# Performance work log

Hardware: AMD Instinct MI355X
Metric: run time of the kernel (lower is better)

The kernel has to match this reference:

```python
import jax, jax.numpy as jnp
import numpy as np
from jax import lax

V, E, H, S, B = 32000, 150, 30, 128, 32
STDV = 1.0 / np.sqrt(30.0)


def setup_inputs() -> dict:
    key = jax.random.key(0)
    ks = jax.random.split(key, 9)
    u = lambda k, shape: jax.random.uniform(k, shape, jnp.float32, -STDV, STDV)
    return {
        "input_batch": jax.random.randint(ks[0], (S, B), 0, V),
        "embedding": u(ks[1], (V, E)),
        "W_ih_lr": u(ks[2], (E + H, H)),
        "b_ih_lr": u(ks[3], (1, H)),
        "W_ih_rl": u(ks[4], (E + H, H)),
        "b_ih_rl": u(ks[5], (1, H)),
        "W_ho": u(ks[6], (2 * H, V)),
        "b_ho": u(ks[7], (1, V)),
        "initial_hidden": u(ks[8], (1, H)),
    }


def reference(input_batch, embedding, W_ih_lr, b_ih_lr, W_ih_rl, b_ih_rl,
              W_ho, b_ho, initial_hidden):
    seq_len, batch = input_batch.shape
    emb = embedding[input_batch]  # (S, B, E)
    # original code detaches the initial hidden state (uses .data)
    init = jnp.broadcast_to(lax.stop_gradient(initial_hidden), (batch, initial_hidden.shape[1]))

    def step(W, b):
        def f(h, w):
            h_new = jnp.tanh(jnp.concatenate([w, h], axis=1) @ W + b)
            return h_new, h_new
        return f

    # forward (left-to-right): f_states[t] = hLR[t+1]
    _, f_states = lax.scan(step(W_ih_lr, b_ih_lr), init, emb)
    # backward (right-to-left) over reversed tokens: r_states[k] = hRL[S-1-k]
    _, r_states = lax.scan(step(W_ih_rl, b_ih_rl), init, emb[::-1])

    # prediction at i uses hLR[i] and hRL[i+1]
    hLR_used = jnp.concatenate([init[None], f_states[:-1]], axis=0)        # hLR[0..S-1]
    hRL_used = jnp.concatenate([r_states[:-1][::-1], init[None]], axis=0)  # hRL[1..S]

    h_cat = jnp.concatenate([hLR_used, hRL_used], axis=-1)  # (S, B, 2H)
    logits = jnp.einsum('sbh,hv->sbv', h_cat, W_ho) + b_ho  # (S, B, V)
    return jax.nn.log_softmax(logits, axis=-1)
```

## Files before the change

kernel.cpp:

```cpp
#include <hip/hip_runtime.h>

#define VSZ 32000
#define ESZ 150
#define HSZ 30
#define SSZ 128
#define BSZ 32
#define SB  4096
#define KP  64

typedef __attribute__((ext_vector_type(8))) short bf16x8;
typedef __attribute__((ext_vector_type(4))) float f32x4;
typedef __attribute__((ext_vector_type(8))) unsigned short u16x8;

static __device__ __forceinline__ unsigned short f2bf(float f) {
  unsigned int u = __float_as_uint(f);
  u += 0x7fffu + ((u >> 16) & 1u);
  return (unsigned short)(u >> 16);
}

static __device__ __forceinline__ float readlane_f(float v, int lane) {
  return __uint_as_float(__builtin_amdgcn_readlane(__float_as_uint(v), lane));
}

__global__ void k_zproj(const int* __restrict__ idx, const float* __restrict__ emb,
                        const float* __restrict__ Wlr, const float* __restrict__ blr,
                        const float* __restrict__ Wrl, const float* __restrict__ brl,
                        float* __restrict__ z) {
  __shared__ float erow[ESZ];
  int tb = blockIdx.x;
  int row = idx[tb];
  for (int i = threadIdx.x; i < ESZ; i += 64) erow[i] = emb[row * ESZ + i];
  __syncthreads();
  int lane = threadIdx.x;
  int j = lane & 31, dir = lane >> 5;
  if (j < HSZ) {
    const float* W = dir ? Wrl : Wlr;
    float acc = dir ? brl[j] : blr[j];
#pragma unroll 10
    for (int e = 0; e < ESZ; ++e) acc = fmaf(erow[e], W[e * HSZ + j], acc);
    z[(dir * SB + tb) * HSZ + j] = acc;
  }
}

__global__ void k_scan(const float* __restrict__ z, const float* __restrict__ Wlr,
                       const float* __restrict__ Wrl, const float* __restrict__ h0,
                       unsigned short* __restrict__ hcat) {
  int j = threadIdx.x;
  int chain = blockIdx.x;
  int dir = chain >> 5, b = chain & 31;
  const float* W = dir ? Wrl : Wlr;
  float w2[HSZ];
#pragma unroll
  for (int k = 0; k < HSZ; ++k) w2[k] = (j < HSZ) ? W[(ESZ + k) * HSZ + j] : 0.f;
  float h = (j < HSZ) ? h0[j] : 0.f;
  bool wr = (j < 32);
  int dim = (j < HSZ) ? dir * HSZ + j : (dir ? 60 : 62) + (j - 30);
  unsigned short padbits = (dim == 60) ? f2bf(1.0f) : (unsigned short)0;
  const float* zc = z + dir * (SB * HSZ) + b * HSZ + j;
  int te0 = dir ? (SSZ - 1) : 0;
  float zv = (j < HSZ) ? zc[te0 * (BSZ * HSZ)] : 0.f;
  for (int t = 0; t < SSZ; ++t) {
    int te = dir ? (SSZ - 1 - t) : t;
    float zn = 0.f;
    if (t < SSZ - 1) {
      int ten = dir ? (SSZ - 2 - t) : (t + 1);
      zn = (j < HSZ) ? zc[ten * (BSZ * HSZ)] : 0.f;
    }
    int r = te * BSZ + b;
    if (wr) hcat[r * KP + dim] = (j < HSZ) ? f2bf(h) : padbits;
    float a0 = zv, a1 = 0.f, a2 = 0.f, a3 = 0.f;
#pragma unroll
    for (int k = 0; k < 28; k += 4) {
      a0 = fmaf(readlane_f(h, k),     w2[k],     a0);
      a1 = fmaf(readlane_f(h, k + 1), w2[k + 1], a1);
      a2 = fmaf(readlane_f(h, k + 2), w2[k + 2], a2);
      a3 = fmaf(readlane_f(h, k + 3), w2[k + 3], a3);
    }
    a0 = fmaf(readlane_f(h, 28), w2[28], a0);
    a1 = fmaf(readlane_f(h, 29), w2[29], a1);
    float x = (a0 + a1) + (a2 + a3);
    float e = __expf(2.0f * x);
    h = 1.0f - __fdividef(2.0f, e + 1.0f);
    zv = zn;
  }
}

__global__ void k_wprep(const float* __restrict__ Who, const float* __restrict__ bho,
                        unsigned short* __restrict__ Wbt) {
  int v = blockIdx.x * 256 + threadIdx.x;
  int kq = blockIdx.y;
  u16x8 pack;
#pragma unroll
  for (int i = 0; i < 8; ++i) {
    int k = kq * 8 + i;
    float val = (k < 60) ? Who[k * VSZ + v] : ((k == 60) ? bho[v] : 0.f);
    pack[i] = f2bf(val);
  }
  *(u16x8*)&Wbt[v * KP + kq * 8] = pack;
}

__global__ void k_sumexp(const unsigned short* __restrict__ hcat,
                         const unsigned short* __restrict__ Wbt,
                         float* __restrict__ part) {
  int mb = blockIdx.x, nb = blockIdx.y;
  int wave = threadIdx.x >> 6, lane = threadIdx.x & 63;
  int g = lane >> 4, c = lane & 15;
  int rbase = mb * 128 + wave * 32;
  bf16x8 bfr[2][2];
#pragma unroll
  for (int rg = 0; rg < 2; ++rg)
#pragma unroll
    for (int ks = 0; ks < 2; ++ks)
      bfr[rg][ks] = *(const bf16x8*)&hcat[(rbase + rg * 16 + c) * KP + ks * 32 + g * 8];
  float se[2] = {0.f, 0.f};
  int c0 = nb * 2000;
  for (int nt = 0; nt < 125; ++nt) {
    int ct = c0 + nt * 16;
    bf16x8 a0 = *(const bf16x8*)&Wbt[(ct + c) * KP + g * 8];
    bf16x8 a1 = *(const bf16x8*)&Wbt[(ct + c) * KP + 32 + g * 8];
#pragma unroll
    for (int rg = 0; rg < 2; ++rg) {
      f32x4 acc = {0.f, 0.f, 0.f, 0.f};
      acc = __builtin_amdgcn_mfma_f32_16x16x32_bf16(a0, bfr[rg][0], acc, 0, 0, 0);
      acc = __builtin_amdgcn_mfma_f32_16x16x32_bf16(a1, bfr[rg][1], acc, 0, 0, 0);
      se[rg] += (__expf(acc[0]) + __expf(acc[1])) + (__expf(acc[2]) + __expf(acc[3]));
    }
  }
#pragma unroll
  for (int rg = 0; rg < 2; ++rg) {
    se[rg] += __shfl_xor(se[rg], 16);
    se[rg] += __shfl_xor(se[rg], 32);
  }
  if (g == 0) {
#pragma unroll
    for (int rg = 0; rg < 2; ++rg)
      part[(rbase + rg * 16 + c) * 16 + nb] = se[rg];
  }
}

__global__ __launch_bounds__(256) void k_writeout(
    const unsigned short* __restrict__ hcat,
    const unsigned short* __restrict__ Wbt,
    const float* __restrict__ part,
    float* __restrict__ out) {
  __shared__ float Lsh[64];
  __shared__ float slab[4][16 * 64];
  int mb = blockIdx.x, nb = blockIdx.y;
  int tid = threadIdx.x;
  if (tid < 64) {
    const float* p = &part[(mb * 64 + tid) * 16];
    float s = 0.f;
#pragma unroll
    for (int k = 0; k < 16; ++k) s += p[k];
    Lsh[tid] = logf(s);
  }
  __syncthreads();
  int wave = tid >> 6, lane = tid & 63;
  int g = lane >> 4, c = lane & 15;
  int row0 = mb * 64 + wave * 16;
  bf16x8 b0f = *(const bf16x8*)&hcat[(row0 + c) * KP + g * 8];
  bf16x8 b1f = *(const bf16x8*)&hcat[(row0 + c) * KP + 32 + g * 8];
  float L = Lsh[wave * 16 + c];
  float* tl = slab[wave];
  int c0 = nb * 2000;
  for (int gq = 0; gq < 31; ++gq) {
    int ct0 = c0 + gq * 64;
#pragma unroll
    for (int t = 0; t < 4; ++t) {
      int ct = ct0 + t * 16;
      bf16x8 a0 = *(const bf16x8*)&Wbt[(ct + c) * KP + g * 8];
      bf16x8 a1 = *(const bf16x8*)&Wbt[(ct + c) * KP + 32 + g * 8];
      f32x4 acc = {0.f, 0.f, 0.f, 0.f};
      acc = __builtin_amdgcn_mfma_f32_16x16x32_bf16(a0, b0f, acc, 0, 0, 0);
      acc = __builtin_amdgcn_mfma_f32_16x16x32_bf16(a1, b1f, acc, 0, 0, 0);
      f32x4 v;
#pragma unroll
      for (int i = 0; i < 4; ++i) v[i] = acc[i] - L;
      int P = (t * 4 + g) ^ (c & 7);
      *(f32x4*)&tl[c * 64 + P * 4] = v;
    }
#pragma unroll
    for (int j = 0; j < 4; ++j) {
      int rj = 4 * j + g;
      int P = c ^ (rj & 7);
      f32x4 w = *(f32x4*)&tl[rj * 64 + P * 4];
      __builtin_nontemporal_store(w, (f32x4*)&out[(row0 + rj) * VSZ + ct0 + c * 4]);
    }
  }
  {
    int ct = c0 + 1984;
    bf16x8 a0 = *(const bf16x8*)&Wbt[(ct + c) * KP + g * 8];
    bf16x8 a1 = *(const bf16x8*)&Wbt[(ct + c) * KP + 32 + g * 8];
    f32x4 acc = {0.f, 0.f, 0.f, 0.f};
    acc = __builtin_amdgcn_mfma_f32_16x16x32_bf16(a0, b0f, acc, 0, 0, 0);
    acc = __builtin_amdgcn_mfma_f32_16x16x32_bf16(a1, b1f, acc, 0, 0, 0);
    f32x4 v;
#pragma unroll
    for (int i = 0; i < 4; ++i) v[i] = acc[i] - L;
    *(f32x4*)&out[(row0 + c) * VSZ + ct + g * 4] = v;
  }
}

extern "C" void kernel_launch(void* const* d_in, const int* in_sizes, int n_in,
                              void* d_out, int out_size, void* d_ws, size_t ws_size,
                              hipStream_t stream) {
  (void)in_sizes; (void)n_in; (void)out_size; (void)ws_size;
  const int*   idx = (const int*)d_in[0];
  const float* emb = (const float*)d_in[1];
  const float* Wlr = (const float*)d_in[2];
  const float* blr = (const float*)d_in[3];
  const float* Wrl = (const float*)d_in[4];
  const float* brl = (const float*)d_in[5];
  const float* Who = (const float*)d_in[6];
  const float* bho = (const float*)d_in[7];
  const float* h0  = (const float*)d_in[8];
  float* out = (float*)d_out;

  char* ws = (char*)d_ws;
  float*          z    = (float*)(ws + 0);
  unsigned short* hcat = (unsigned short*)(ws + 983040);
  unsigned short* Wbt  = (unsigned short*)(ws + 1507328);
  float*          part = (float*)(ws + 5603328);

  k_zproj<<<SB, 64, 0, stream>>>(idx, emb, Wlr, blr, Wrl, brl, z);
  k_scan<<<64, 64, 0, stream>>>(z, Wlr, Wrl, h0, hcat);
  k_wprep<<<dim3(125, 8), 256, 0, stream>>>(Who, bho, Wbt);
  k_sumexp<<<dim3(32, 16), 256, 0, stream>>>(hcat, Wbt, part);
  k_writeout<<<dim3(64, 16), 256, 0, stream>>>(hcat, Wbt, part, out);
}
```

Baseline: 274.9 us.

## Fuse sum-exp and writeout kernels with per-row-block atomic grid barrier

Merges the log-sum-exp partial pass and the output writeout into one kernel. The 16 column blocks that share a row block publish their partial sums and then spin on an atomic counter until all have arrived. Each block then reuses its register-held hcat fragments to recompute the logits and write the outputs. This removes one kernel launch and the reload of hcat. The cost is a cross-block spin wait that relies on all 16 cooperating blocks being resident at once (512 blocks, 2 per CU via launch bounds), plus a small extra kernel to zero the counters.

```diff
diff --git a/kernel.cpp b/kernel.cpp
--- a/kernel.cpp
+++ b/kernel.cpp
@@ -20,6 +20,10 @@
 
 static __device__ __forceinline__ float readlane_f(float v, int lane) {
   return __uint_as_float(__builtin_amdgcn_readlane(__float_as_uint(v), lane));
+}
+
+__global__ void k_zeroflags(int* __restrict__ cnt) {
+  if (threadIdx.x < 32) cnt[threadIdx.x] = 0;
 }
 
 __global__ void k_zproj(const int* __restrict__ idx, const float* __restrict__ emb,
@@ -99,11 +103,15 @@
   *(u16x8*)&Wbt[v * KP + kq * 8] = pack;
 }
 
-__global__ void k_sumexp(const unsigned short* __restrict__ hcat,
-                         const unsigned short* __restrict__ Wbt,
-                         float* __restrict__ part) {
-  int mb = blockIdx.x, nb = blockIdx.y;
-  int wave = threadIdx.x >> 6, lane = threadIdx.x & 63;
+__global__ __launch_bounds__(256, 2) void k_fused(
+    const unsigned short* __restrict__ hcat,
+    const unsigned short* __restrict__ Wbt,
+    float* __restrict__ part, int* __restrict__ cnt,
+    float* __restrict__ out) {
+  __shared__ float slab[4][16 * 64];
+  int nb = blockIdx.x, mb = blockIdx.y;
+  int tid = threadIdx.x;
+  int wave = tid >> 6, lane = tid & 63;
   int g = lane >> 4, c = lane & 15;
   int rbase = mb * 128 + wave * 32;
   bf16x8 bfr[2][2];
@@ -112,8 +120,8 @@
 #pragma unroll
     for (int ks = 0; ks < 2; ++ks)
       bfr[rg][ks] = *(const bf16x8*)&hcat[(rbase + rg * 16 + c) * KP + ks * 32 + g * 8];
+  int c0 = nb * 2000;
   float se[2] = {0.f, 0.f};
-  int c0 = nb * 2000;
   for (int nt = 0; nt < 125; ++nt) {
     int ct = c0 + nt * 16;
     bf16x8 a0 = *(const bf16x8*)&Wbt[(ct + c) * KP + g * 8];
@@ -134,40 +142,57 @@
   if (g == 0) {
 #pragma unroll
     for (int rg = 0; rg < 2; ++rg)
-      part[(rbase + rg * 16 + c) * 16 + nb] = se[rg];
-  }
-}
-
-__global__ __launch_bounds__(256) void k_writeout(
-    const unsigned short* __restrict__ hcat,
-    const unsigned short* __restrict__ Wbt,
-    const float* __restrict__ part,
-    float* __restrict__ out) {
-  __shared__ float Lsh[64];
-  __shared__ float slab[4][16 * 64];
-  int mb = blockIdx.x, nb = blockIdx.y;
-  int tid = threadIdx.x;
-  if (tid < 64) {
-    const float* p = &part[(mb * 64 + tid) * 16];
+      __hip_atomic_store(&part[(rbase + rg * 16 + c) * 16 + nb], se[rg],
+                         __ATOMIC_RELAXED, __HIP_MEMORY_SCOPE_AGENT);
+  }
+  __syncthreads();
+  if (tid == 0) {
+    __hip_atomic_fetch_add(&cnt[mb], 1, __ATOMIC_ACQ_REL, __HIP_MEMORY_SCOPE_AGENT);
+    while (__hip_atomic_load(&cnt[mb], __ATOMIC_ACQUIRE, __HIP_MEMORY_SCOPE_AGENT) < 16) {}
+  }
+  __syncthreads();
+  float L[2];
+#pragma unroll
+  for (int rg = 0; rg < 2; ++rg) {
+    const float* p = &part[(rbase + rg * 16 + c) * 16];
     float s = 0.f;
 #pragma unroll
-    for (int k = 0; k < 16; ++k) s += p[k];
-    Lsh[tid] = logf(s);
-  }
-  __syncthreads();
-  int wave = tid >> 6, lane = tid & 63;
-  int g = lane >> 4, c = lane & 15;
-  int row0 = mb * 64 + wave * 16;
-  bf16x8 b0f = *(const bf16x8*)&hcat[(row0 + c) * KP + g * 8];
-  bf16x8 b1f = *(const bf16x8*)&hcat[(row0 + c) * KP + 32 + g * 8];
-  float L = Lsh[wave * 16 + c];
+    for (int k = 0; k < 16; ++k)
+      s += __hip_atomic_load(&p[k], __ATOMIC_RELAXED, __HIP_MEMORY_SCOPE_AGENT);
+    L[rg] = logf(s);
+  }
   float* tl = slab[wave];
-  int c0 = nb * 2000;
-  for (int gq = 0; gq < 31; ++gq) {
-    int ct0 = c0 + gq * 64;
-#pragma unroll
-    for (int t = 0; t < 4; ++t) {
-      int ct = ct0 + t * 16;
+#pragma unroll 1
+  for (int rg = 0; rg < 2; ++rg) {
+    int row0 = rbase + rg * 16;
+    bf16x8 b0f = bfr[rg][0], b1f = bfr[rg][1];
+    float Lr = L[rg];
+    for (int gq = 0; gq < 31; ++gq) {
+      int ct0 = c0 + gq * 64;
+#pragma unroll
+      for (int t = 0; t < 4; ++t) {
+        int ct = ct0 + t * 16;
+        bf16x8 a0 = *(const bf16x8*)&Wbt[(ct + c) * KP + g * 8];
+        bf16x8 a1 = *(const bf16x8*)&Wbt[(ct + c) * KP + 32 + g * 8];
+        f32x4 acc = {0.f, 0.f, 0.f, 0.f};
+        acc = __builtin_amdgcn_mfma_f32_16x16x32_bf16(a0, b0f, acc, 0, 0, 0);
+        acc = __builtin_amdgcn_mfma_f32_16x16x32_bf16(a1, b1f, acc, 0, 0, 0);
+        f32x4 v;
+#pragma unroll
+        for (int i = 0; i < 4; ++i) v[i] = acc[i] - Lr;
+        int P = (t * 4 + g) ^ (c & 7);
+        *(f32x4*)&tl[c * 64 + P * 4] = v;
+      }
+#pragma unroll
+      for (int j = 0; j < 4; ++j) {
+        int rj = 4 * j + g;
+        int P = c ^ (rj & 7);
+        f32x4 w = *(f32x4*)&tl[rj * 64 + P * 4];
+        __builtin_nontemporal_store(w, (f32x4*)&out[(row0 + rj) * VSZ + ct0 + c * 4]);
+      }
+    }
+    {
+      int ct = c0 + 1984;
       bf16x8 a0 = *(const bf16x8*)&Wbt[(ct + c) * KP + g * 8];
       bf16x8 a1 = *(const bf16x8*)&Wbt[(ct + c) * KP + 32 + g * 8];
       f32x4 acc = {0.f, 0.f, 0.f, 0.f};
@@ -175,29 +200,9 @@
       acc = __builtin_amdgcn_mfma_f32_16x16x32_bf16(a1, b1f, acc, 0, 0, 0);
       f32x4 v;
 #pragma unroll
-      for (int i = 0; i < 4; ++i) v[i] = acc[i] - L;
-      int P = (t * 4 + g) ^ (c & 7);
-      *(f32x4*)&tl[c * 64 + P * 4] = v;
-    }
-#pragma unroll
-    for (int j = 0; j < 4; ++j) {
-      int rj = 4 * j + g;
-      int P = c ^ (rj & 7);
-      f32x4 w = *(f32x4*)&tl[rj * 64 + P * 4];
-      __builtin_nontemporal_store(w, (f32x4*)&out[(row0 + rj) * VSZ + ct0 + c * 4]);
-    }
-  }
-  {
-    int ct = c0 + 1984;
-    bf16x8 a0 = *(const bf16x8*)&Wbt[(ct + c) * KP + g * 8];
-    bf16x8 a1 = *(const bf16x8*)&Wbt[(ct + c) * KP + 32 + g * 8];
-    f32x4 acc = {0.f, 0.f, 0.f, 0.f};
-    acc = __builtin_amdgcn_mfma_f32_16x16x32_bf16(a0, b0f, acc, 0, 0, 0);
-    acc = __builtin_amdgcn_mfma_f32_16x16x32_bf16(a1, b1f, acc, 0, 0, 0);
-    f32x4 v;
-#pragma unroll
-    for (int i = 0; i < 4; ++i) v[i] = acc[i] - L;
-    *(f32x4*)&out[(row0 + c) * VSZ + ct + g * 4] = v;
+      for (int i = 0; i < 4; ++i) v[i] = acc[i] - Lr;
+      *(f32x4*)&out[(row0 + c) * VSZ + ct + g * 4] = v;
+    }
   }
 }
 
@@ -221,10 +226,11 @@
   unsigned short* hcat = (unsigned short*)(ws + 983040);
   unsigned short* Wbt  = (unsigned short*)(ws + 1507328);
   float*          part = (float*)(ws + 5603328);
-
+  int*            cnt  = (int*)(ws + 5865472);
+
+  k_zeroflags<<<1, 64, 0, stream>>>(cnt);
   k_zproj<<<SB, 64, 0, stream>>>(idx, emb, Wlr, blr, Wrl, brl, z);
   k_scan<<<64, 64, 0, stream>>>(z, Wlr, Wrl, h0, hcat);
   k_wprep<<<dim3(125, 8), 256, 0, stream>>>(Who, bho, Wbt);
-  k_sumexp<<<dim3(32, 16), 256, 0, stream>>>(hcat, Wbt, part);
-  k_writeout<<<dim3(64, 16), 256, 0, stream>>>(hcat, Wbt, part, out);
-}
+  k_fused<<<dim3(16, 32), 256, 0, stream>>>(hcat, Wbt, part, cnt, out);
+}
```

Result: slower. 298.1 us (+8.5%).
